# Performance work log

Measured on AMD Instinct MI355X. Metric: run time of the kernel, lower is better.

The kernel has to match this reference:

```python
import jax, jax.numpy as jnp
import numpy as np

EPS = 1e-8


def _gmm_params(points, gamma):
    # points: (B,N,3), gamma: (B,N,K)
    pi = jnp.mean(gamma, axis=1)                       # (B,K)
    # fused weighted-mean reduction; avoids the (B,N,K,3) broadcast intermediate
    weighted_sum = jnp.einsum('bnk,bnd->bkd', gamma, points)  # (B,K,3)
    mu = weighted_sum / (pi[..., None] + EPS)          # (B,K,3)
    return pi, mu


def _rigid_transform(mu_s, pi_s, mu_t, pi_t):
    # weighted Procrustes: min_{R,t} sum_k w_k ||R mu_s_k + t - mu_t_k||^2
    w = pi_s * pi_t                                    # (B,K)
    w_sum = jnp.sum(w, axis=1, keepdims=True) + EPS    # (B,1)
    c_s = jnp.einsum('bk,bkd->bd', w, mu_s) / w_sum    # (B,3)
    c_t = jnp.einsum('bk,bkd->bd', w, mu_t) / w_sum    # (B,3)
    s_c = mu_s - c_s[:, None, :]                       # (B,K,3)
    t_c = mu_t - c_t[:, None, :]
    # weighted covariance H = sum_k w_k s_k t_k^T  -> (B,3,3)
    H = jnp.einsum('bk,bki,bkj->bij', w, s_c, t_c)
    U, S, Vh = jnp.linalg.svd(H)                       # batched tiny 3x3 SVD
    V = jnp.swapaxes(Vh, -1, -2)
    Ut = jnp.swapaxes(U, -1, -2)
    det = jnp.linalg.det(jnp.matmul(V, Ut))            # (B,)
    # reflection correction: R = V diag(1,1,det) U^T (scale last column of V)
    corr = jnp.stack([jnp.ones_like(det), jnp.ones_like(det), det], axis=-1)  # (B,3)
    R = jnp.matmul(V * corr[:, None, :], Ut)           # (B,3,3)
    t = c_t - jnp.einsum('bij,bj->bi', R, c_s)         # (B,3)
    return R, t


def setup_inputs() -> dict:
    key = jax.random.key(0)
    k1, k2, k3, k4 = jax.random.split(key, 4)
    B, N, K = 32, 16384, 64
    points_x = jax.random.normal(k1, (B, N, 3), dtype=jnp.float32)
    points_y = jax.random.normal(k2, (B, N, 3), dtype=jnp.float32)
    # responsibilities: rows over K sum to 1 (as from an E-step softmax)
    gamma_x = jax.nn.softmax(jax.random.normal(k3, (B, N, K), dtype=jnp.float32), axis=-1)
    gamma_y = jax.nn.softmax(jax.random.normal(k4, (B, N, K), dtype=jnp.float32), axis=-1)
    return {"points_x": points_x, "points_y": points_y, "gamma_x": gamma_x, "gamma_y": gamma_y}


def reference(points_x, points_y, gamma_x, gamma_y):
    pi_x, mu_x = _gmm_params(points_x, gamma_x)
    pi_y, mu_y = _gmm_params(points_y, gamma_y)
    R, t = _rigid_transform(mu_x, pi_x, mu_y, pi_y)
    return (R, t)
```

## Files before the change

kernel.cpp:

```cpp
#include <hip/hip_runtime.h>
#include <math.h>

constexpr int Bb = 32;
constexpr int Nn = 16384;
constexpr int Kk = 64;
constexpr int NCHUNK = 8;
constexpr int ROWS = Nn / NCHUNK;
constexpr int NBLK1 = 2 * Bb * NCHUNK;
#define EPSF 1e-8f

__global__ __launch_bounds__(256) void gmm_partial_kernel(
    const float* __restrict__ points_x, const float* __restrict__ points_y,
    const float* __restrict__ gamma_x,  const float* __restrict__ gamma_y,
    float4* __restrict__ ws4)
{
    const int bx    = blockIdx.x;
    const int chunk = bx & (NCHUNK - 1);
    const int combo = bx >> 3;
    const int s     = combo >> 5;
    const int b     = combo & 31;

    const float* __restrict__ gbase = (s ? gamma_y : gamma_x) + (size_t)b * Nn * Kk;
    const float* __restrict__ pbase = (s ? points_y : points_x) + (size_t)b * Nn * 3;

    const int tid  = threadIdx.x;
    const int wave = tid >> 6;
    const int lane = tid & 63;
    const int sub  = lane >> 4;
    const int kq   = lane & 15;

    float a0=0.f,a1=0.f,a2=0.f,a3=0.f;
    float x0=0.f,x1=0.f,x2=0.f,x3=0.f;
    float y0=0.f,y1=0.f,y2=0.f,y3=0.f;
    float z0=0.f,z1=0.f,z2=0.f,z3=0.f;

    const int row0 = chunk * ROWS;
    for (int r = wave * 4; r < ROWS; r += 16) {
        const int n = row0 + r + sub;
        const float4 g = *reinterpret_cast<const float4*>(
            gbase + (size_t)n * Kk + (kq << 2));
        const float ppx = pbase[n * 3 + 0];
        const float ppy = pbase[n * 3 + 1];
        const float ppz = pbase[n * 3 + 2];
        a0 += g.x; x0 = fmaf(g.x, ppx, x0); y0 = fmaf(g.x, ppy, y0); z0 = fmaf(g.x, ppz, z0);
        a1 += g.y; x1 = fmaf(g.y, ppx, x1); y1 = fmaf(g.y, ppy, y1); z1 = fmaf(g.y, ppz, z1);
        a2 += g.z; x2 = fmaf(g.z, ppx, x2); y2 = fmaf(g.z, ppy, y2); z2 = fmaf(g.z, ppz, z2);
        a3 += g.w; x3 = fmaf(g.w, ppx, x3); y3 = fmaf(g.w, ppy, y3); z3 = fmaf(g.w, ppz, z3);
    }

#define RED2(v) { v += __shfl_xor(v, 16); v += __shfl_xor(v, 32); }
    RED2(a0) RED2(a1) RED2(a2) RED2(a3)
    RED2(x0) RED2(x1) RED2(x2) RED2(x3)
    RED2(y0) RED2(y1) RED2(y2) RED2(y3)
    RED2(z0) RED2(z1) RED2(z2) RED2(z3)
#undef RED2

    __shared__ float4 lds[4][Kk];
    if (lane < 16) {
        lds[wave][kq * 4 + 0] = make_float4(a0, x0, y0, z0);
        lds[wave][kq * 4 + 1] = make_float4(a1, x1, y1, z1);
        lds[wave][kq * 4 + 2] = make_float4(a2, x2, y2, z2);
        lds[wave][kq * 4 + 3] = make_float4(a3, x3, y3, z3);
    }
    __syncthreads();
    if (tid < Kk) {
        float4 v0 = lds[0][tid], v1 = lds[1][tid], v2 = lds[2][tid], v3 = lds[3][tid];
        float4 o;
        o.x = v0.x + v1.x + v2.x + v3.x;
        o.y = v0.y + v1.y + v2.y + v3.y;
        o.z = v0.z + v1.z + v2.z + v3.z;
        o.w = v0.w + v1.w + v2.w + v3.w;
        ws4[(size_t)bx * Kk + tid] = o;
    }
}

__device__ __forceinline__ float wred64(float v) {
    v += __shfl_xor(v, 1);  v += __shfl_xor(v, 2);  v += __shfl_xor(v, 4);
    v += __shfl_xor(v, 8);  v += __shfl_xor(v, 16); v += __shfl_xor(v, 32);
    return v;
}

__global__ __launch_bounds__(64) void gmm_finalize_kernel(
    const float4* __restrict__ ws4, float* __restrict__ out)
{
    const int b = blockIdx.x;
    const int k = threadIdx.x;

    float4 s0 = make_float4(0.f, 0.f, 0.f, 0.f);
    float4 s1 = make_float4(0.f, 0.f, 0.f, 0.f);
    for (int c = 0; c < NCHUNK; ++c) {
        float4 t0 = ws4[((size_t)(b * NCHUNK + c)) * Kk + k];
        float4 t1 = ws4[((size_t)((Bb + b) * NCHUNK + c)) * Kk + k];
        s0.x += t0.x; s0.y += t0.y; s0.z += t0.z; s0.w += t0.w;
        s1.x += t1.x; s1.y += t1.y; s1.z += t1.z; s1.w += t1.w;
    }

    const float pix = s0.x * (1.f / Nn);
    const float piy = s1.x * (1.f / Nn);
    const float idx_ = 1.f / (pix + EPSF);
    const float idy_ = 1.f / (piy + EPSF);
    const float mux0 = s0.y * idx_, mux1 = s0.z * idx_, mux2 = s0.w * idx_;
    const float muy0 = s1.y * idy_, muy1 = s1.z * idy_, muy2 = s1.w * idy_;
    const float w = pix * piy;

    const float wsum = wred64(w) + EPSF;
    const float cs0 = wred64(w * mux0) / wsum;
    const float cs1 = wred64(w * mux1) / wsum;
    const float cs2 = wred64(w * mux2) / wsum;
    const float ct0 = wred64(w * muy0) / wsum;
    const float ct1 = wred64(w * muy1) / wsum;
    const float ct2 = wred64(w * muy2) / wsum;

    const float sx0 = mux0 - cs0, sx1 = mux1 - cs1, sx2 = mux2 - cs2;
    const float tx0 = muy0 - ct0, tx1 = muy1 - ct1, tx2 = muy2 - ct2;

    float H[3][3];
    H[0][0] = wred64(w * sx0 * tx0); H[0][1] = wred64(w * sx0 * tx1); H[0][2] = wred64(w * sx0 * tx2);
    H[1][0] = wred64(w * sx1 * tx0); H[1][1] = wred64(w * sx1 * tx1); H[1][2] = wred64(w * sx1 * tx2);
    H[2][0] = wred64(w * sx2 * tx0); H[2][1] = wred64(w * sx2 * tx1); H[2][2] = wred64(w * sx2 * tx2);

    if (k != 0) return;

    float R_[3][3];
    float tv[3];

    float mx = 0.f;
    for (int i = 0; i < 3; ++i)
        for (int j = 0; j < 3; ++j) mx = fmaxf(mx, fabsf(H[i][j]));

    if (mx < 1e-35f) {
        for (int i = 0; i < 3; ++i)
            for (int j = 0; j < 3; ++j) R_[i][j] = (i == j) ? 1.f : 0.f;
        tv[0] = ct0 - cs0; tv[1] = ct1 - cs1; tv[2] = ct2 - cs2;
    } else {
        const float inv = 1.f / mx;
        float h[3][3];
        for (int i = 0; i < 3; ++i)
            for (int j = 0; j < 3; ++j) h[i][j] = H[i][j] * inv;

        float A[3][3];
        for (int i = 0; i < 3; ++i)
            for (int j = 0; j < 3; ++j) {
                float acc = 0.f;
                for (int m = 0; m < 3; ++m) acc += h[m][i] * h[m][j];
                A[i][j] = acc;
            }

        float V[3][3] = {{1.f,0.f,0.f},{0.f,1.f,0.f},{0.f,0.f,1.f}};
        const int PQ[3][2] = {{0,1},{0,2},{1,2}};
        for (int sweep = 0; sweep < 15; ++sweep) {
            for (int pi_ = 0; pi_ < 3; ++pi_) {
                const int p = PQ[pi_][0], q = PQ[pi_][1];
                const float apq = A[p][q];
                if (fabsf(apq) < 1e-20f) continue;
                const float theta = (A[q][q] - A[p][p]) / (2.f * apq);
                const float tt = copysignf(1.f, theta) /
                                 (fabsf(theta) + sqrtf(theta * theta + 1.f));
                const float c = 1.f / sqrtf(tt * tt + 1.f);
                const float sn = tt * c;
                for (int r = 0; r < 3; ++r) {
                    const float arp = A[r][p], arq = A[r][q];
                    A[r][p] = c * arp - sn * arq;
                    A[r][q] = sn * arp + c * arq;
                }
                for (int r = 0; r < 3; ++r) {
                    const float apr = A[p][r], aqr = A[q][r];
                    A[p][r] = c * apr - sn * aqr;
                    A[q][r] = sn * apr + c * aqr;
                }
                for (int r = 0; r < 3; ++r) {
                    const float vrp = V[r][p], vrq = V[r][q];
                    V[r][p] = c * vrp - sn * vrq;
                    V[r][q] = sn * vrp + c * vrq;
                }
            }
        }

        float lam[3] = {A[0][0], A[1][1], A[2][2]};
        for (int a2 = 0; a2 < 2; ++a2)
            for (int b2 = a2 + 1; b2 < 3; ++b2)
                if (lam[b2] > lam[a2]) {
                    float tmp = lam[a2]; lam[a2] = lam[b2]; lam[b2] = tmp;
                    for (int r = 0; r < 3; ++r) {
                        float tv2 = V[r][a2]; V[r][a2] = V[r][b2]; V[r][b2] = tv2;
                    }
                }

        float U[3][3], sig[3];
        for (int c2 = 0; c2 < 3; ++c2) {
            float u[3];
            for (int i = 0; i < 3; ++i)
                u[i] = h[i][0] * V[0][c2] + h[i][1] * V[1][c2] + h[i][2] * V[2][c2];
            sig[c2] = sqrtf(fmaxf(u[0]*u[0] + u[1]*u[1] + u[2]*u[2], 0.f));
            const float is = 1.f / fmaxf(sig[c2], 1e-30f);
            for (int i = 0; i < 3; ++i) U[i][c2] = u[i] * is;
        }
        if (sig[2] < 1e-6f * sig[0]) {
            float u2[3] = {
                U[1][0] * U[2][1] - U[2][0] * U[1][1],
                U[2][0] * U[0][1] - U[0][0] * U[2][1],
                U[0][0] * U[1][1] - U[1][0] * U[0][1]};
            const float nn2 = sqrtf(u2[0]*u2[0] + u2[1]*u2[1] + u2[2]*u2[2]);
            const float is = 1.f / fmaxf(nn2, 1e-30f);
            for (int i = 0; i < 3; ++i) U[i][2] = u2[i] * is;
        }

        const float detU =
            U[0][0] * (U[1][1] * U[2][2] - U[2][1] * U[1][2]) -
            U[0][1] * (U[1][0] * U[2][2] - U[2][0] * U[1][2]) +
            U[0][2] * (U[1][0] * U[2][1] - U[2][0] * U[1][1]);
        const float detV =
            V[0][0] * (V[1][1] * V[2][2] - V[2][1] * V[1][2]) -
            V[0][1] * (V[1][0] * V[2][2] - V[2][0] * V[1][2]) +
            V[0][2] * (V[1][0] * V[2][1] - V[2][0] * V[1][1]);
        const float d = (detU * detV < 0.f) ? -1.f : 1.f;

        for (int i = 0; i < 3; ++i)
            for (int j = 0; j < 3; ++j)
                R_[i][j] = V[i][0] * U[j][0] + V[i][1] * U[j][1] + d * V[i][2] * U[j][2];

        tv[0] = ct0 - (R_[0][0] * cs0 + R_[0][1] * cs1 + R_[0][2] * cs2);
        tv[1] = ct1 - (R_[1][0] * cs0 + R_[1][1] * cs1 + R_[1][2] * cs2);
        tv[2] = ct2 - (R_[2][0] * cs0 + R_[2][1] * cs1 + R_[2][2] * cs2);
    }

    for (int i = 0; i < 3; ++i)
        for (int j = 0; j < 3; ++j)
            out[b * 9 + i * 3 + j] = R_[i][j];
    for (int i = 0; i < 3; ++i)
        out[Bb * 9 + b * 3 + i] = tv[i];
}

extern "C" void kernel_launch(void* const* d_in, const int* in_sizes, int n_in,
                              void* d_out, int out_size, void* d_ws, size_t ws_size,
                              hipStream_t stream) {
    const float* points_x = (const float*)d_in[0];
    const float* points_y = (const float*)d_in[1];
    const float* gamma_x  = (const float*)d_in[2];
    const float* gamma_y  = (const float*)d_in[3];
    float* out = (float*)d_out;
    float4* ws4 = (float4*)d_ws;

    gmm_partial_kernel<<<NBLK1, 256, 0, stream>>>(
        points_x, points_y, gamma_x, gamma_y, ws4);
    gmm_finalize_kernel<<<Bb, 64, 0, stream>>>(ws4, out);
}
```

Before: 310.2 us.

## Split rows into more chunks, stage points in LDS, unroll two rows per iteration

New measurement: 310.2 us. No clear change (-0.0%).

```diff
diff --git a/kernel.cpp b/kernel.cpp
--- a/kernel.cpp
+++ b/kernel.cpp
@@ -4,19 +4,19 @@
 constexpr int Bb = 32;
 constexpr int Nn = 16384;
 constexpr int Kk = 64;
-constexpr int NCHUNK = 8;
-constexpr int ROWS = Nn / NCHUNK;
-constexpr int NBLK1 = 2 * Bb * NCHUNK;
 #define EPSF 1e-8f
 
+template <int NCH>
 __global__ __launch_bounds__(256) void gmm_partial_kernel(
     const float* __restrict__ points_x, const float* __restrict__ points_y,
     const float* __restrict__ gamma_x,  const float* __restrict__ gamma_y,
     float4* __restrict__ ws4)
 {
+    constexpr int ROWSC = Nn / NCH;
+
     const int bx    = blockIdx.x;
-    const int chunk = bx & (NCHUNK - 1);
-    const int combo = bx >> 3;
+    const int chunk = bx % NCH;
+    const int combo = bx / NCH;
     const int s     = combo >> 5;
     const int b     = combo & 31;
 
@@ -29,23 +29,42 @@
     const int sub  = lane >> 4;
     const int kq   = lane & 15;
 
+    const int row0 = chunk * ROWSC;
+
+    __shared__ float pts[ROWSC * 3];
+    {
+        const float4* __restrict__ psrc =
+            reinterpret_cast<const float4*>(pbase + (size_t)row0 * 3);
+        float4* pdst = reinterpret_cast<float4*>(pts);
+        constexpr int NV4 = ROWSC * 3 / 4;
+        for (int i = tid; i < NV4; i += 256) pdst[i] = psrc[i];
+    }
+    __syncthreads();
+
     float a0=0.f,a1=0.f,a2=0.f,a3=0.f;
     float x0=0.f,x1=0.f,x2=0.f,x3=0.f;
     float y0=0.f,y1=0.f,y2=0.f,y3=0.f;
     float z0=0.f,z1=0.f,z2=0.f,z3=0.f;
 
-    const int row0 = chunk * ROWS;
-    for (int r = wave * 4; r < ROWS; r += 16) {
-        const int n = row0 + r + sub;
-        const float4 g = *reinterpret_cast<const float4*>(
-            gbase + (size_t)n * Kk + (kq << 2));
-        const float ppx = pbase[n * 3 + 0];
-        const float ppy = pbase[n * 3 + 1];
-        const float ppz = pbase[n * 3 + 2];
-        a0 += g.x; x0 = fmaf(g.x, ppx, x0); y0 = fmaf(g.x, ppy, y0); z0 = fmaf(g.x, ppz, z0);
-        a1 += g.y; x1 = fmaf(g.y, ppx, x1); y1 = fmaf(g.y, ppy, y1); z1 = fmaf(g.y, ppz, z1);
-        a2 += g.z; x2 = fmaf(g.z, ppx, x2); y2 = fmaf(g.z, ppy, y2); z2 = fmaf(g.z, ppz, z2);
-        a3 += g.w; x3 = fmaf(g.w, ppx, x3); y3 = fmaf(g.w, ppy, y3); z3 = fmaf(g.w, ppz, z3);
+    for (int r = wave * 8; r < ROWSC; r += 32) {
+        const int n0 = r + sub;
+        const int n1 = r + 4 + sub;
+        const float4 g0 = *reinterpret_cast<const float4*>(
+            gbase + (size_t)(row0 + n0) * Kk + (kq << 2));
+        const float4 g1 = *reinterpret_cast<const float4*>(
+            gbase + (size_t)(row0 + n1) * Kk + (kq << 2));
+        const float px0 = pts[n0*3+0], py0 = pts[n0*3+1], pz0 = pts[n0*3+2];
+        const float px1 = pts[n1*3+0], py1 = pts[n1*3+1], pz1 = pts[n1*3+2];
+
+        a0 += g0.x; x0 = fmaf(g0.x, px0, x0); y0 = fmaf(g0.x, py0, y0); z0 = fmaf(g0.x, pz0, z0);
+        a1 += g0.y; x1 = fmaf(g0.y, px0, x1); y1 = fmaf(g0.y, py0, y1); z1 = fmaf(g0.y, pz0, z1);
+        a2 += g0.z; x2 = fmaf(g0.z, px0, x2); y2 = fmaf(g0.z, py0, y2); z2 = fmaf(g0.z, pz0, z2);
+        a3 += g0.w; x3 = fmaf(g0.w, px0, x3); y3 = fmaf(g0.w, py0, y3); z3 = fmaf(g0.w, pz0, z3);
+
+        a0 += g1.x; x0 = fmaf(g1.x, px1, x0); y0 = fmaf(g1.x, py1, y0); z0 = fmaf(g1.x, pz1, z0);
+        a1 += g1.y; x1 = fmaf(g1.y, px1, x1); y1 = fmaf(g1.y, py1, y1); z1 = fmaf(g1.y, pz1, z1);
+        a2 += g1.z; x2 = fmaf(g1.z, px1, x2); y2 = fmaf(g1.z, py1, y2); z2 = fmaf(g1.z, pz1, z2);
+        a3 += g1.w; x3 = fmaf(g1.w, px1, x3); y3 = fmaf(g1.w, py1, y3); z3 = fmaf(g1.w, pz1, z3);
     }
 
 #define RED2(v) { v += __shfl_xor(v, 16); v += __shfl_xor(v, 32); }
@@ -81,16 +100,16 @@
 }
 
 __global__ __launch_bounds__(64) void gmm_finalize_kernel(
-    const float4* __restrict__ ws4, float* __restrict__ out)
+    const float4* __restrict__ ws4, float* __restrict__ out, int nchunk)
 {
     const int b = blockIdx.x;
     const int k = threadIdx.x;
 
     float4 s0 = make_float4(0.f, 0.f, 0.f, 0.f);
     float4 s1 = make_float4(0.f, 0.f, 0.f, 0.f);
-    for (int c = 0; c < NCHUNK; ++c) {
-        float4 t0 = ws4[((size_t)(b * NCHUNK + c)) * Kk + k];
-        float4 t1 = ws4[((size_t)((Bb + b) * NCHUNK + c)) * Kk + k];
+    for (int c = 0; c < nchunk; ++c) {
+        float4 t0 = ws4[((size_t)(b * nchunk + c)) * Kk + k];
+        float4 t1 = ws4[((size_t)((Bb + b) * nchunk + c)) * Kk + k];
         s0.x += t0.x; s0.y += t0.y; s0.z += t0.z; s0.w += t0.w;
         s1.x += t1.x; s1.y += t1.y; s1.z += t1.z; s1.w += t1.w;
     }
@@ -241,7 +260,14 @@
     float* out = (float*)d_out;
     float4* ws4 = (float4*)d_ws;
 
-    gmm_partial_kernel<<<NBLK1, 256, 0, stream>>>(
-        points_x, points_y, gamma_x, gamma_y, ws4);
-    gmm_finalize_kernel<<<Bb, 64, 0, stream>>>(ws4, out);
-}
+    const size_t need32 = (size_t)2 * Bb * 32 * Kk * sizeof(float4);
+    if (ws_size >= need32) {
+        gmm_partial_kernel<32><<<2 * Bb * 32, 256, 0, stream>>>(
+            points_x, points_y, gamma_x, gamma_y, ws4);
+        gmm_finalize_kernel<<<Bb, 64, 0, stream>>>(ws4, out, 32);
+    } else {
+        gmm_partial_kernel<8><<<2 * Bb * 8, 256, 0, stream>>>(
+            points_x, points_y, gamma_x, gamma_y, ws4);
+        gmm_finalize_kernel<<<Bb, 64, 0, stream>>>(ws4, out, 8);
+    }
+}
```
